# Kernel optimization log

Measured on AMD Instinct MI355X. Metric: run time of the kernel, lower is better.

Reference implementation:

```python
import jax, jax.numpy as jnp
import numpy as np
import math

B, S, HID, NH, HD = 2, 1024, 768, 12, 64
MAXP = 1024  # max_position_embeddings


def setup_inputs() -> dict:
    key = jax.random.key(0)
    ks = jax.random.split(key, 12)
    s = 0.02
    return {
        "hidden_states": jax.random.normal(ks[0], (B, S, HID), jnp.float32),
        "attention_mask": jnp.zeros((B, 1, 1, S), jnp.float32),
        "scaled_attention_mask": jax.random.uniform(ks[1], (1, 1, S, S), dtype=jnp.float32),
        "selector_outputs": jax.random.uniform(ks[2], (B, 1, S, 1), dtype=jnp.float32),
        "Wq": jax.random.normal(ks[3], (HID, HID), jnp.float32) * s,
        "bq": jnp.zeros((HID,), jnp.float32),
        "Wk": jax.random.normal(ks[4], (HID, HID), jnp.float32) * s,
        "bk": jnp.zeros((HID,), jnp.float32),
        "Wv": jax.random.normal(ks[5], (HID, HID), jnp.float32) * s,
        "bv": jnp.zeros((HID,), jnp.float32),
        "dist_emb": jax.random.normal(ks[6], (2 * MAXP - 1, HD), jnp.float32) * s,
    }


def _heads(x):
    # [B,S,HID] -> [B,NH,S,HD]
    return x.reshape(B, S, NH, HD).transpose(0, 2, 1, 3)


def reference(hidden_states, attention_mask, scaled_attention_mask, selector_outputs,
              Wq, bq, Wk, bk, Wv, bv, dist_emb):
    q = _heads(hidden_states @ Wq + bq)  # [B,NH,S,HD]
    k = _heads(hidden_states @ Wk + bk)
    v = _heads(hidden_states @ Wv + bv)

    scores = jnp.einsum('bhld,bhrd->bhlr', q, k)  # [B,NH,S,S]

    # relative_key positional bias
    pos = jnp.arange(S)
    dist_idx = pos[:, None] - pos[None, :] + (MAXP - 1)  # [S,S] in [0, 2*MAXP-2]
    pos_emb = dist_emb[dist_idx]  # [S,S,HD]
    scores = scores + jnp.einsum('bhld,lrd->bhlr', q, pos_emb)

    scores = scores / math.sqrt(HD)
    scores = scores + attention_mask  # additive mask (global branch)

    probs = jax.nn.softmax(scores, axis=-1)  # dropout prob = 0.0 -> identity
    context = jnp.einsum('bhlr,bhrd->bhld', probs, v)

    # local (selector-gated) branch; note: attention_mask added a second time,
    # faithful to the original code
    scores_l = scores * scaled_attention_mask + attention_mask
    probs_l = jax.nn.softmax(scores_l, axis=-1)
    local_context = jnp.einsum('bhlr,bhrd->bhld', probs_l, v)

    sel = selector_outputs  # [B,1,S,1]
    context = sel * local_context + (1.0 - sel) * context  # [B,NH,S,HD]

    # [B,NH,S,HD] -> [B,S,HID]
    return context.transpose(0, 2, 1, 3).reshape(B, S, HID)
```

## Files before the change

kernel.cpp:

```cpp
#include <hip/hip_runtime.h>
#include <hip/hip_bf16.h>
#include <math.h>

#define BB   2
#define SS   1024
#define HIDD 768
#define NHH  12
#define HDD  64

typedef float f32x4 __attribute__((ext_vector_type(4)));
typedef short bf8   __attribute__((ext_vector_type(8)));
typedef unsigned short u16;
typedef unsigned int u32;
typedef u16 u16x8 __attribute__((ext_vector_type(8)));
typedef u16 u16x4 __attribute__((ext_vector_type(4)));

__device__ __forceinline__ u16 f2bf(float x) {
  unsigned int u = __float_as_uint(x);
  u += 0x7fffu + ((u >> 16) & 1u);
  return (u16)(u >> 16);
}
__device__ __forceinline__ float bf2f(u16 x) {
  return __uint_as_float(((u32)x) << 16);
}

__device__ __forceinline__ bf8 ldfrag(const u16* t, int row, int kc) {
  return *(const bf8*)&t[row * 64 + (kc ^ ((row & 7) << 3))];
}

__global__ __launch_bounds__(256) void xconv_kernel(const float* __restrict__ X,
                                                    u16* __restrict__ Xb) {
  int i = (blockIdx.x * 256 + threadIdx.x) * 8;
  float4 a = *(const float4*)&X[i];
  float4 b = *(const float4*)&X[i + 4];
  u16x8 o;
  o[0] = f2bf(a.x); o[1] = f2bf(a.y); o[2] = f2bf(a.z); o[3] = f2bf(a.w);
  o[4] = f2bf(b.x); o[5] = f2bf(b.y); o[6] = f2bf(b.z); o[7] = f2bf(b.w);
  *(u16x8*)&Xb[i] = o;
}

__global__ __launch_bounds__(256) void wtconv_kernel(
    const float* __restrict__ Wq, const float* __restrict__ Wk,
    const float* __restrict__ Wv, u16* __restrict__ Wt) {
  const int zi = blockIdx.z;
  const float* __restrict__ W = (zi == 0) ? Wq : (zi == 1 ? Wk : Wv);
  const int n0 = blockIdx.x * 64;
  const int k0 = blockIdx.y * 64;
  __shared__ float t[64][65];
  const int tid = threadIdx.x;
  {
    const int kl = tid >> 4;
    const int nl = (tid & 15) * 4;
#pragma unroll
    for (int p = 0; p < 4; ++p) {
      float4 v = *(const float4*)&W[(size_t)(k0 + kl + 16 * p) * HIDD + n0 + nl];
      t[kl + 16 * p][nl + 0] = v.x;
      t[kl + 16 * p][nl + 1] = v.y;
      t[kl + 16 * p][nl + 2] = v.z;
      t[kl + 16 * p][nl + 3] = v.w;
    }
  }
  __syncthreads();
  {
    const int nl = tid >> 4;
    const int cl = (tid & 15) * 4;
#pragma unroll
    for (int p = 0; p < 4; ++p) {
      const int n = nl + 16 * p;
      u16x4 o;
      o[0] = f2bf(t[cl + 0][n]);
      o[1] = f2bf(t[cl + 1][n]);
      o[2] = f2bf(t[cl + 2][n]);
      o[3] = f2bf(t[cl + 3][n]);
      *(u16x4*)&Wt[(size_t)(zi * HIDD + n0 + n) * HIDD + k0 + cl] = o;
    }
  }
}

__global__ __launch_bounds__(256) void econv_kernel(const float* __restrict__ demb,
                                                    u16* __restrict__ eb) {
  int i = (blockIdx.x * 256 + threadIdx.x) * 8;
  if (i < 2047 * HDD) {
    float4 a = *(const float4*)&demb[i];
    float4 b = *(const float4*)&demb[i + 4];
    u16x8 o;
    o[0] = f2bf(a.x); o[1] = f2bf(a.y); o[2] = f2bf(a.z); o[3] = f2bf(a.w);
    o[4] = f2bf(b.x); o[5] = f2bf(b.y); o[6] = f2bf(b.z); o[7] = f2bf(b.w);
    *(u16x8*)&eb[i] = o;
  }
}

__global__ __launch_bounds__(256) void sconv_kernel(const float* __restrict__ sm,
                                                    u16* __restrict__ smb) {
  int i = (blockIdx.x * 256 + threadIdx.x) * 8;
  float4 a = *(const float4*)&sm[i];
  float4 b = *(const float4*)&sm[i + 4];
  u16x8 o;
  o[0] = f2bf(a.x); o[1] = f2bf(a.y); o[2] = f2bf(a.z); o[3] = f2bf(a.w);
  o[4] = f2bf(b.x); o[5] = f2bf(b.y); o[6] = f2bf(b.z); o[7] = f2bf(b.w);
  *(u16x8*)&smb[i] = o;
}

__global__ __launch_bounds__(256) void qkv_mfma_kernel(
    const u16* __restrict__ Xb,
    const u16* __restrict__ Wt,
    const float* __restrict__ bq, const float* __restrict__ bk,
    const float* __restrict__ bv,
    u16* __restrict__ qb, u16* __restrict__ kb, u16* __restrict__ vt) {
  const int bn = blockIdx.x;
  const int bm = blockIdx.y;
  const int zi = bn / 6;

  __shared__ u16 As[64 * 64];
  __shared__ u16 Bs[128 * 64];

  const int tid  = threadIdx.x;
  const int lane = tid & 63;
  const int w    = tid >> 6;
  const int g    = lane >> 4;
  const int ln   = lane & 15;
  const int wm   = (w >> 1) * 32;
  const int wn   = (w & 1) * 64;

  f32x4 acc[2][4] = {};

  const int srow = tid >> 3;
  const int scol = (tid & 7) * 8;
  const u16* Ag = Xb + (size_t)(bm * 64 + srow) * HIDD + scol;
  const u16* Bg = Wt + (size_t)(bn * 128 + srow) * HIDD + scol;

  for (int k0 = 0; k0 < HIDD; k0 += 64) {
    if (k0) __syncthreads();
#pragma unroll
    for (int p = 0; p < 2; ++p) {
      const int r = srow + 32 * p;
      const int sw = (r & 7) << 3;
      *(u16x8*)&As[r * 64 + (scol ^ sw)] =
          *(const u16x8*)&Ag[(size_t)(32 * p) * HIDD + k0];
    }
#pragma unroll
    for (int p = 0; p < 4; ++p) {
      const int r = srow + 32 * p;
      const int sw = (r & 7) << 3;
      *(u16x8*)&Bs[r * 64 + (scol ^ sw)] =
          *(const u16x8*)&Bg[(size_t)(32 * p) * HIDD + k0];
    }
    __syncthreads();

    bf8 af[2][2], bfr[4][2];
#pragma unroll
    for (int f = 0; f < 2; ++f)
#pragma unroll
      for (int kk = 0; kk < 2; ++kk)
        af[f][kk] = ldfrag(As, wm + 16 * f + ln, kk * 32 + g * 8);
#pragma unroll
    for (int f = 0; f < 4; ++f)
#pragma unroll
      for (int kk = 0; kk < 2; ++kk)
        bfr[f][kk] = ldfrag(Bs, wn + 16 * f + ln, kk * 32 + g * 8);
    if (zi < 2) {
#pragma unroll
      for (int mf = 0; mf < 2; ++mf)
#pragma unroll
        for (int nf = 0; nf < 4; ++nf)
#pragma unroll
          for (int kk = 0; kk < 2; ++kk)
            acc[mf][nf] = __builtin_amdgcn_mfma_f32_16x16x32_bf16(
                bfr[nf][kk], af[mf][kk], acc[mf][nf], 0, 0, 0);
    } else {
#pragma unroll
      for (int mf = 0; mf < 2; ++mf)
#pragma unroll
        for (int nf = 0; nf < 4; ++nf)
#pragma unroll
          for (int kk = 0; kk < 2; ++kk)
            acc[mf][nf] = __builtin_amdgcn_mfma_f32_16x16x32_bf16(
                af[mf][kk], bfr[nf][kk], acc[mf][nf], 0, 0, 0);
    }
  }

  const int mrow  = bm * 64 + wm;
  const int nbase = (bn % 6) * 128 + wn;
  const int h     = nbase >> 6;

  if (zi < 2) {
    const float* __restrict__ bias = zi ? bk : bq;
    u16* __restrict__ outp = zi ? kb : qb;
#pragma unroll
    for (int nf = 0; nf < 4; ++nf) {
      const int d0 = 16 * nf + 4 * g;
      float4 bi = *(const float4*)&bias[nbase + d0];
#pragma unroll
      for (int mf = 0; mf < 2; ++mf) {
        const int m = mrow + 16 * mf + ln;
        const int b = m >> 10, s = m & 1023;
        u16x4 o;
        o[0] = f2bf(acc[mf][nf][0] + bi.x);
        o[1] = f2bf(acc[mf][nf][1] + bi.y);
        o[2] = f2bf(acc[mf][nf][2] + bi.z);
        o[3] = f2bf(acc[mf][nf][3] + bi.w);
        *(u16x4*)&outp[(((size_t)(b * NHH + h)) * SS + s) * HDD + d0] = o;
      }
    }
  } else {
#pragma unroll
    for (int nf = 0; nf < 4; ++nf) {
      const int d = 16 * nf + ln;
      const float bi = bv[nbase + d];
#pragma unroll
      for (int mf = 0; mf < 2; ++mf) {
        const int m = mrow + 16 * mf + 4 * g;
        const int b = m >> 10, s = m & 1023;
        u16x4 o;
        o[0] = f2bf(acc[mf][nf][0] + bi);
        o[1] = f2bf(acc[mf][nf][1] + bi);
        o[2] = f2bf(acc[mf][nf][2] + bi);
        o[3] = f2bf(acc[mf][nf][3] + bi);
        *(u16x4*)&vt[(((size_t)(b * NHH + h)) * HDD + d) * SS + s] = o;
      }
    }
  }
}

__global__ __launch_bounds__(256, 3) void attn_kernel(
    const u16* __restrict__ qbg,
    const u16* __restrict__ kbg,
    const u16* __restrict__ vtg,
    const u16* __restrict__ eb,
    const float* __restrict__ am,
    const u16* __restrict__ smb,
    const float* __restrict__ selp,
    float* __restrict__ out) {
  const int bid  = blockIdx.x;
  const int xcd  = bid & 7;
  const int idx  = bid >> 3;
  const int inner = idx & 31;
  const int grp  = idx >> 5;
  const int hg   = grp * 8 + xcd;
  const int h    = hg % NHH;
  const int b    = hg / NHH;
  const int l0   = inner * 32;

  const int bh = b * NHH + h;
  const size_t hoff = (size_t)bh * SS * HDD;

  __shared__ __align__(16) u16 smbuf[16384];
  __shared__ __align__(4)  u16 tbuf[4 * 80 * 20];

  const int tid  = threadIdx.x;
  const int lane = tid & 63;
  const int w    = tid >> 6;
  const int p    = w >> 1;
  const int wp   = w & 1;
  const int g    = lane >> 4;
  const int ln   = lane & 15;

  u16* ksw = smbuf + p * 4096;
  u16* vsw = smbuf + 8192 + p * 4096;
  u16* Tw  = tbuf + w * (80 * 20);

  bf8 qf[2];
  {
    const u16* qp = qbg + hoff + (size_t)(l0 + 16 * wp + ln) * HDD + g * 8;
    qf[0] = *(const bf8*)(qp);
    qf[1] = *(const bf8*)(qp + 32);
  }

  f32x4 acc1[4] = {}, acc2[4] = {};
  float m1 = -INFINITY, m2 = -INFINITY, sum1 = 0.f, sum2 = 0.f;

  const int tid128 = tid & 127;
  const int rr = tid128 >> 2;
  const int cc = (tid128 & 3) << 4;
  const int S0i = ((lane & 16) << 1) | ln;
  const int S1i = S0i + 16;
  const bool ghi = (lane & 32) != 0;

  const u16* kgp0 = kbg + hoff;
  const u16* vgp0 = vtg + hoff;

  u16x8 kr[2][2], vr[2][2];
  {
    const int r0 = 512 * p;
#pragma unroll
    for (int pp = 0; pp < 2; ++pp) {
      const int r = rr + 32 * pp;
      kr[pp][0] = *(const u16x8*)&kgp0[(size_t)(r0 + r) * HDD + cc];
      kr[pp][1] = *(const u16x8*)&kgp0[(size_t)(r0 + r) * HDD + cc + 8];
      vr[pp][0] = *(const u16x8*)&vgp0[(size_t)r * SS + r0 + cc];
      vr[pp][1] = *(const u16x8*)&vgp0[(size_t)r * SS + r0 + cc + 8];
    }
  }

  for (int t = 0; t < 8; ++t) {
    const int r0 = 512 * p + 64 * t;

    const int W0 = l0 + 16 * wp - r0 + 960;
    bf8 ef[5][2];
#pragma unroll
    for (int c5 = 0; c5 < 5; ++c5) {
      const int gr = min(W0 + 16 * c5 + ln, 2046);
      const u16* ep = eb + (size_t)gr * HDD + g * 8;
      ef[c5][0] = *(const bf8*)(ep);
      ef[c5][1] = *(const bf8*)(ep + 32);
    }
    f32x4 amv[4];
    u16x4 smv[4];
#pragma unroll
    for (int ct = 0; ct < 4; ++ct) {
      amv[ct] = *(const f32x4*)&am[(b << 10) + r0 + 16 * ct + 4 * g];
      smv[ct] = *(const u16x4*)&smb[(size_t)(l0 + 16 * wp + ln) * SS +
                                    r0 + 16 * ct + 4 * g];
    }

    __syncthreads();
#pragma unroll
    for (int pp = 0; pp < 2; ++pp) {
      const int r = rr + 32 * pp;
      const int sw = (r & 7) << 3;
      *(u16x8*)&ksw[r * 64 + (cc ^ sw)] = kr[pp][0];
      *(u16x8*)&ksw[r * 64 + ((cc + 8) ^ sw)] = kr[pp][1];
      *(u16x8*)&vsw[r * 64 + (cc ^ sw)] = vr[pp][0];
      *(u16x8*)&vsw[r * 64 + ((cc + 8) ^ sw)] = vr[pp][1];
    }
    __syncthreads();

    if (t < 7) {
      const int rn = r0 + 64;
#pragma unroll
      for (int pp = 0; pp < 2; ++pp) {
        const int r = rr + 32 * pp;
        kr[pp][0] = *(const u16x8*)&kgp0[(size_t)(rn + r) * HDD + cc];
        kr[pp][1] = *(const u16x8*)&kgp0[(size_t)(rn + r) * HDD + cc + 8];
        vr[pp][0] = *(const u16x8*)&vgp0[(size_t)r * SS + rn + cc];
        vr[pp][1] = *(const u16x8*)&vgp0[(size_t)r * SS + rn + cc + 8];
      }
    }

    __builtin_amdgcn_s_setprio(1);
#pragma unroll
    for (int c5 = 0; c5 < 5; ++c5) {
      f32x4 x = {0.f, 0.f, 0.f, 0.f};
      x = __builtin_amdgcn_mfma_f32_16x16x32_bf16(ef[c5][0], qf[0], x, 0, 0, 0);
      x = __builtin_amdgcn_mfma_f32_16x16x32_bf16(ef[c5][1], qf[1], x, 0, 0, 0);
#pragma unroll
      for (int i = 0; i < 4; ++i)
        Tw[(16 * c5 + 4 * g + i) * 20 + ln] = f2bf(x[i]);
    }
    f32x4 sc[4];
#pragma unroll
    for (int ct = 0; ct < 4; ++ct) {
      f32x4 x = {0.f, 0.f, 0.f, 0.f};
#pragma unroll
      for (int kk = 0; kk < 2; ++kk)
        x = __builtin_amdgcn_mfma_f32_16x16x32_bf16(
            ldfrag(ksw, ct * 16 + ln, kk * 32 + g * 8), qf[kk], x, 0, 0, 0);
      sc[ct] = x;
    }
    __builtin_amdgcn_s_setprio(0);

    float s1r[4][4], s2r[4][4];
#pragma unroll
    for (int ct = 0; ct < 4; ++ct)
#pragma unroll
      for (int i = 0; i < 4; ++i) {
        const int e = ln + 63 - 16 * ct - 4 * g - i;
        const float tb = bf2f(Tw[e * 20 + ln]);
        const float s1 = (sc[ct][i] + tb) * 0.125f + amv[ct][i];
        s1r[ct][i] = s1;
        s2r[ct][i] = s1 * bf2f(smv[ct][i]) + amv[ct][i];
      }

    bf8 pa1[2], pa2[2];
    {
      float mx = s1r[0][0];
#pragma unroll
      for (int ct = 0; ct < 4; ++ct)
#pragma unroll
        for (int i = 0; i < 4; ++i) mx = fmaxf(mx, s1r[ct][i]);
      mx = fmaxf(mx, __shfl_xor(mx, 16, 64));
      mx = fmaxf(mx, __shfl_xor(mx, 32, 64));
      const float mn = fmaxf(m1, mx);
      const float scl = __expf(m1 - mn);
      m1 = mn;
      float rs = 0.f;
      u32 pk[4][2];
#pragma unroll
      for (int ct = 0; ct < 4; ++ct) {
        const float p0 = __expf(s1r[ct][0] - mn);
        const float p1 = __expf(s1r[ct][1] - mn);
        const float p2 = __expf(s1r[ct][2] - mn);
        const float p3 = __expf(s1r[ct][3] - mn);
        rs += (p0 + p1) + (p2 + p3);
        pk[ct][0] = (u32)f2bf(p0) | ((u32)f2bf(p1) << 16);
        pk[ct][1] = (u32)f2bf(p2) | ((u32)f2bf(p3) << 16);
      }
      rs += __shfl_xor(rs, 16, 64);
      rs += __shfl_xor(rs, 32, 64);
      sum1 = sum1 * scl + rs;
#pragma unroll
      for (int i = 0; i < 4; ++i) {
        const float s = __shfl(scl, (lane & 48) + 4 * g + i, 64);
#pragma unroll
        for (int dt = 0; dt < 4; ++dt) acc1[dt][i] *= s;
      }
#pragma unroll
      for (int kk = 0; kk < 2; ++kk) {
        union { u32 u[4]; bf8 v; } f;
        const int cA = 2 * kk, cB = 2 * kk + 1;
        u32 a, bb;
        a = (u32)__shfl((int)pk[cA][0], S0i, 64);
        bb = (u32)__shfl((int)pk[cB][0], S0i, 64);
        f.u[0] = ghi ? bb : a;
        a = (u32)__shfl((int)pk[cA][1], S0i, 64);
        bb = (u32)__shfl((int)pk[cB][1], S0i, 64);
        f.u[1] = ghi ? bb : a;
        a = (u32)__shfl((int)pk[cA][0], S1i, 64);
        bb = (u32)__shfl((int)pk[cB][0], S1i, 64);
        f.u[2] = ghi ? bb : a;
        a = (u32)__shfl((int)pk[cA][1], S1i, 64);
        bb = (u32)__shfl((int)pk[cB][1], S1i, 64);
        f.u[3] = ghi ? bb : a;
        pa1[kk] = f.v;
      }
    }
    {
      float mx = s2r[0][0];
#pragma unroll
      for (int ct = 0; ct < 4; ++ct)
#pragma unroll
        for (int i = 0; i < 4; ++i) mx = fmaxf(mx, s2r[ct][i]);
      mx = fmaxf(mx, __shfl_xor(mx, 16, 64));
      mx = fmaxf(mx, __shfl_xor(mx, 32, 64));
      const float mn = fmaxf(m2, mx);
      const float scl = __expf(m2 - mn);
      m2 = mn;
      float rs = 0.f;
      u32 pk[4][2];
#pragma unroll
      for (int ct = 0; ct < 4; ++ct) {
        const float p0 = __expf(s2r[ct][0] - mn);
        const float p1 = __expf(s2r[ct][1] - mn);
        const float p2 = __expf(s2r[ct][2] - mn);
        const float p3 = __expf(s2r[ct][3] - mn);
        rs += (p0 + p1) + (p2 + p3);
        pk[ct][0] = (u32)f2bf(p0) | ((u32)f2bf(p1) << 16);
        pk[ct][1] = (u32)f2bf(p2) | ((u32)f2bf(p3) << 16);
      }
      rs += __shfl_xor(rs, 16, 64);
      rs += __shfl_xor(rs, 32, 64);
      sum2 = sum2 * scl + rs;
#pragma unroll
      for (int i = 0; i < 4; ++i) {
        const float s = __shfl(scl, (lane & 48) + 4 * g + i, 64);
#pragma unroll
        for (int dt = 0; dt < 4; ++dt) acc2[dt][i] *= s;
      }
#pragma unroll
      for (int kk = 0; kk < 2; ++kk) {
        union { u32 u[4]; bf8 v; } f;
        const int cA = 2 * kk, cB = 2 * kk + 1;
        u32 a, bb;
        a = (u32)__shfl((int)pk[cA][0], S0i, 64);
        bb = (u32)__shfl((int)pk[cB][0], S0i, 64);
        f.u[0] = ghi ? bb : a;
        a = (u32)__shfl((int)pk[cA][1], S0i, 64);
        bb = (u32)__shfl((int)pk[cB][1], S0i, 64);
        f.u[1] = ghi ? bb : a;
        a = (u32)__shfl((int)pk[cA][0], S1i, 64);
        bb = (u32)__shfl((int)pk[cB][0], S1i, 64);
        f.u[2] = ghi ? bb : a;
        a = (u32)__shfl((int)pk[cA][1], S1i, 64);
        bb = (u32)__shfl((int)pk[cB][1], S1i, 64);
        f.u[3] = ghi ? bb : a;
        pa2[kk] = f.v;
      }
    }

    __builtin_amdgcn_s_setprio(1);
#pragma unroll
    for (int kk = 0; kk < 2; ++kk) {
#pragma unroll
      for (int dt = 0; dt < 4; ++dt) {
        bf8 vb = ldfrag(vsw, dt * 16 + ln, kk * 32 + g * 8);
        acc1[dt] = __builtin_amdgcn_mfma_f32_16x16x32_bf16(pa1[kk], vb, acc1[dt], 0, 0, 0);
        acc2[dt] = __builtin_amdgcn_mfma_f32_16x16x32_bf16(pa2[kk], vb, acc2[dt], 0, 0, 0);
      }
    }
    __builtin_amdgcn_s_setprio(0);
  }

  __syncthreads();
  float* scr = (float*)smbuf;
  if (p == 1) {
#pragma unroll
    for (int i = 0; i < 4; ++i) {
      const int row = 4 * g + i;
#pragma unroll
      for (int dt = 0; dt < 4; ++dt) {
        scr[wp * 1024 + row * 64 + dt * 16 + ln] = acc1[dt][i];
        scr[2048 + wp * 1024 + row * 64 + dt * 16 + ln] = acc2[dt][i];
      }
    }
    if (g == 0) {
      const int sb = 4096 + (wp * 16 + ln) * 4;
      scr[sb + 0] = m1;
      scr[sb + 1] = sum1;
      scr[sb + 2] = m2;
      scr[sb + 3] = sum2;
    }
  }
  __syncthreads();
  if (p == 0) {
    const int sb = 4096 + (wp * 16 + ln) * 4;
    const float mB1 = scr[sb + 0], sB1 = scr[sb + 1];
    const float mB2 = scr[sb + 2], sB2 = scr[sb + 3];
    const float M1 = fmaxf(m1, mB1);
    const float e1A = __expf(m1 - M1), e1B = __expf(mB1 - M1);
    const float inv1 = 1.f / (sum1 * e1A + sB1 * e1B);
    const float a1 = e1A * inv1, c1 = e1B * inv1;
    const float M2 = fmaxf(m2, mB2);
    const float e2A = __expf(m2 - M2), e2B = __expf(mB2 - M2);
    const float inv2 = 1.f / (sum2 * e2A + sB2 * e2B);
    const float a2 = e2A * inv2, c2 = e2B * inv2;
#pragma unroll
    for (int i = 0; i < 4; ++i) {
      const int src = (lane & 48) + 4 * g + i;
      const float a1s = __shfl(a1, src, 64), c1s = __shfl(c1, src, 64);
      const float a2s = __shfl(a2, src, 64), c2s = __shfl(c2, src, 64);
      const int row = 4 * g + i;
      const int lg = l0 + 16 * wp + row;
      const float se = selp[(b << 10) + lg];
#pragma unroll
      for (int dt = 0; dt < 4; ++dt) {
        const float aB1 = scr[wp * 1024 + row * 64 + dt * 16 + ln];
        const float aB2 = scr[2048 + wp * 1024 + row * 64 + dt * 16 + ln];
        const float o1 = acc1[dt][i] * a1s + aB1 * c1s;
        const float o2 = acc2[dt][i] * a2s + aB2 * c2s;
        out[((size_t)((b << 10) + lg)) * HIDD + h * HDD + dt * 16 + ln] =
            se * o2 + (1.f - se) * o1;
      }
    }
  }
}

extern "C" void kernel_launch(void* const* d_in, const int* in_sizes, int n_in,
                              void* d_out, int out_size, void* d_ws, size_t ws_size,
                              hipStream_t stream) {
  const float* hidden = (const float*)d_in[0];
  const float* am     = (const float*)d_in[1];
  const float* smask  = (const float*)d_in[2];
  const float* selp   = (const float*)d_in[3];
  const float* Wq     = (const float*)d_in[4];
  const float* bq     = (const float*)d_in[5];
  const float* Wk     = (const float*)d_in[6];
  const float* bk     = (const float*)d_in[7];
  const float* Wv     = (const float*)d_in[8];
  const float* bv     = (const float*)d_in[9];
  const float* demb   = (const float*)d_in[10];
  float* out = (float*)d_out;

  u16* wsp = (u16*)d_ws;
  const size_t NEL = (size_t)BB * NHH * SS * HDD;
  u16* Xb  = wsp;
  u16* Wt  = Xb + (size_t)2048 * HIDD;
  u16* qbw = Wt + (size_t)3 * HIDD * HIDD;
  u16* kbw = qbw + NEL;
  u16* vtw = kbw + NEL;
  u16* ebw = vtw + NEL;
  u16* smb = ebw + (size_t)2047 * HDD;

  xconv_kernel<<<768, 256, 0, stream>>>(hidden, Xb);
  dim3 gw(HIDD / 64, HIDD / 64, 3);
  wtconv_kernel<<<gw, 256, 0, stream>>>(Wq, Wk, Wv, Wt);
  econv_kernel<<<64, 256, 0, stream>>>(demb, ebw);
  sconv_kernel<<<512, 256, 0, stream>>>(smask, smb);

  dim3 g1(18, 32);
  qkv_mfma_kernel<<<g1, 256, 0, stream>>>(Xb, Wt, bq, bk, bv, qbw, kbw, vtw);

  attn_kernel<<<768, 256, 0, stream>>>(qbw, kbw, vtw, ebw, am, smb, selp, out);
}
```

Before: 105.5 us.

## Precompute relative-position bias in separate kernel and restructure attention with per-wave tiles

Moves the q·dist_emb relative-position bias into a separate tbias_kernel that writes a bf16 [B,NH,S,S] bias tensor to global memory. The attention kernel then streams that tensor instead of recomputing it with MFMAs. The attention kernel also changes: each wave gets its own private LDS K/V tiles of 32 keys, which removes the block-wide __syncthreads, and it register-prefetches the next tile. It adds a lazy softmax rescale that skips it when the running max grows by at most 8, and defers the row-sum shuffles to the end. The cost is an extra 48MB bias write and read through global memory.

Result: slower. 166.7 us (+58.0%).

```diff
diff --git a/kernel.cpp b/kernel.cpp
--- a/kernel.cpp
+++ b/kernel.cpp
@@ -222,11 +222,56 @@
   }
 }
 
+__global__ __launch_bounds__(256) void tbias_kernel(
+    const u16* __restrict__ qbg,
+    const u16* __restrict__ eb,
+    u16* __restrict__ Tg) {
+  const int bh = blockIdx.z;
+  const int l0 = blockIdx.y * 16;
+  const int tid = threadIdx.x;
+  const int lane = tid & 63;
+  const int w = tid >> 6;
+  const int g = lane >> 4;
+  const int ln = lane & 15;
+  const int r0 = (blockIdx.x * 4 + w) * 64;
+
+  __shared__ u16 tb[4][80 * 20];
+  u16* Tw = tb[w];
+
+  const u16* qp = qbg + ((size_t)bh * SS + l0 + ln) * HDD + g * 8;
+  const bf8 qf0 = *(const bf8*)qp;
+  const bf8 qf1 = *(const bf8*)(qp + 32);
+
+  const int W0 = l0 - r0 + 960;
+#pragma unroll
+  for (int c5 = 0; c5 < 5; ++c5) {
+    const int gr = min(max(W0 + 16 * c5 + ln, 0), 2046);
+    const u16* ep = eb + (size_t)gr * HDD + g * 8;
+    f32x4 x = {0.f, 0.f, 0.f, 0.f};
+    x = __builtin_amdgcn_mfma_f32_16x16x32_bf16(*(const bf8*)ep, qf0, x, 0, 0, 0);
+    x = __builtin_amdgcn_mfma_f32_16x16x32_bf16(*(const bf8*)(ep + 32), qf1, x, 0, 0, 0);
+#pragma unroll
+    for (int i = 0; i < 4; ++i)
+      Tw[(16 * c5 + 4 * g + i) * 20 + ln] = f2bf(x[i]);
+  }
+#pragma unroll
+  for (int ct = 0; ct < 4; ++ct) {
+    const int E0 = ln + 63 - 16 * ct - 4 * g;
+    u16x4 o;
+    o[0] = Tw[(E0 - 0) * 20 + ln];
+    o[1] = Tw[(E0 - 1) * 20 + ln];
+    o[2] = Tw[(E0 - 2) * 20 + ln];
+    o[3] = Tw[(E0 - 3) * 20 + ln];
+    __builtin_nontemporal_store(
+        o, (u16x4*)&Tg[((size_t)bh * SS + l0 + ln) * SS + r0 + 16 * ct + 4 * g]);
+  }
+}
+
 __global__ __launch_bounds__(256, 3) void attn_kernel(
     const u16* __restrict__ qbg,
     const u16* __restrict__ kbg,
     const u16* __restrict__ vtg,
-    const u16* __restrict__ eb,
+    const u16* __restrict__ Tg,
     const float* __restrict__ am,
     const u16* __restrict__ smb,
     const float* __restrict__ selp,
@@ -245,7 +290,6 @@
   const size_t hoff = (size_t)bh * SS * HDD;
 
   __shared__ __align__(16) u16 smbuf[16384];
-  __shared__ __align__(4)  u16 tbuf[4 * 80 * 20];
 
   const int tid  = threadIdx.x;
   const int lane = tid & 63;
@@ -255,101 +299,75 @@
   const int g    = lane >> 4;
   const int ln   = lane & 15;
 
-  u16* ksw = smbuf + p * 4096;
-  u16* vsw = smbuf + 8192 + p * 4096;
-  u16* Tw  = tbuf + w * (80 * 20);
-
+  u16* ksw = smbuf + w * 4096;
+  u16* vsw = ksw + 2048;
+
+  const int lq = l0 + 16 * wp + ln;
   bf8 qf[2];
   {
-    const u16* qp = qbg + hoff + (size_t)(l0 + 16 * wp + ln) * HDD + g * 8;
-    qf[0] = *(const bf8*)(qp);
+    const u16* qp = qbg + hoff + (size_t)lq * HDD + g * 8;
+    qf[0] = *(const bf8*)qp;
     qf[1] = *(const bf8*)(qp + 32);
   }
 
   f32x4 acc1[4] = {}, acc2[4] = {};
   float m1 = -INFINITY, m2 = -INFINITY, sum1 = 0.f, sum2 = 0.f;
 
-  const int tid128 = tid & 127;
-  const int rr = tid128 >> 2;
-  const int cc = (tid128 & 3) << 4;
-  const int S0i = ((lane & 16) << 1) | ln;
-  const int S1i = S0i + 16;
-  const bool ghi = (lane & 32) != 0;
-
-  const u16* kgp0 = kbg + hoff;
-  const u16* vgp0 = vtg + hoff;
-
-  u16x8 kr[2][2], vr[2][2];
+  const int srow = lane & 31;
+  const int sh   = (lane >> 5) * 32;
+  const int kx   = (srow & 7) << 3;
+  const int vrow = lane;
+  const int vx   = (vrow & 3) << 3;
+
+  const u16* kgp = kbg + hoff;
+  const u16* vgp = vtg + hoff + (size_t)vrow * SS;
+  const u16* Trow = Tg + ((size_t)bh * SS + lq) * SS;
+  const u16* Srow = smb + (size_t)lq * SS;
+  const float* Arow = am + (b << 10);
+
+  const int S0base = 16 * ((2 * g) & 3) + ln;
+  const int S1base = 16 * ((2 * g + 1) & 3) + ln;
+  const bool gh = (lane & 32) != 0;
+
+  u16x8 kq[4], vq[4];
+  u16x4 tbq[2], smq[2];
+  f32x4 amq[2];
   {
     const int r0 = 512 * p;
-#pragma unroll
-    for (int pp = 0; pp < 2; ++pp) {
-      const int r = rr + 32 * pp;
-      kr[pp][0] = *(const u16x8*)&kgp0[(size_t)(r0 + r) * HDD + cc];
-      kr[pp][1] = *(const u16x8*)&kgp0[(size_t)(r0 + r) * HDD + cc + 8];
-      vr[pp][0] = *(const u16x8*)&vgp0[(size_t)r * SS + r0 + cc];
-      vr[pp][1] = *(const u16x8*)&vgp0[(size_t)r * SS + r0 + cc + 8];
-    }
-  }
-
-  for (int t = 0; t < 8; ++t) {
-    const int r0 = 512 * p + 64 * t;
-
-    const int W0 = l0 + 16 * wp - r0 + 960;
-    bf8 ef[5][2];
-#pragma unroll
-    for (int c5 = 0; c5 < 5; ++c5) {
-      const int gr = min(W0 + 16 * c5 + ln, 2046);
-      const u16* ep = eb + (size_t)gr * HDD + g * 8;
-      ef[c5][0] = *(const bf8*)(ep);
-      ef[c5][1] = *(const bf8*)(ep + 32);
-    }
-    f32x4 amv[4];
-    u16x4 smv[4];
-#pragma unroll
-    for (int ct = 0; ct < 4; ++ct) {
-      amv[ct] = *(const f32x4*)&am[(b << 10) + r0 + 16 * ct + 4 * g];
-      smv[ct] = *(const u16x4*)&smb[(size_t)(l0 + 16 * wp + ln) * SS +
-                                    r0 + 16 * ct + 4 * g];
-    }
-
-    __syncthreads();
-#pragma unroll
-    for (int pp = 0; pp < 2; ++pp) {
-      const int r = rr + 32 * pp;
-      const int sw = (r & 7) << 3;
-      *(u16x8*)&ksw[r * 64 + (cc ^ sw)] = kr[pp][0];
-      *(u16x8*)&ksw[r * 64 + ((cc + 8) ^ sw)] = kr[pp][1];
-      *(u16x8*)&vsw[r * 64 + (cc ^ sw)] = vr[pp][0];
-      *(u16x8*)&vsw[r * 64 + ((cc + 8) ^ sw)] = vr[pp][1];
-    }
-    __syncthreads();
-
-    if (t < 7) {
-      const int rn = r0 + 64;
-#pragma unroll
-      for (int pp = 0; pp < 2; ++pp) {
-        const int r = rr + 32 * pp;
-        kr[pp][0] = *(const u16x8*)&kgp0[(size_t)(rn + r) * HDD + cc];
-        kr[pp][1] = *(const u16x8*)&kgp0[(size_t)(rn + r) * HDD + cc + 8];
-        vr[pp][0] = *(const u16x8*)&vgp0[(size_t)r * SS + rn + cc];
-        vr[pp][1] = *(const u16x8*)&vgp0[(size_t)r * SS + rn + cc + 8];
-      }
-    }
-
-    __builtin_amdgcn_s_setprio(1);
-#pragma unroll
-    for (int c5 = 0; c5 < 5; ++c5) {
-      f32x4 x = {0.f, 0.f, 0.f, 0.f};
-      x = __builtin_amdgcn_mfma_f32_16x16x32_bf16(ef[c5][0], qf[0], x, 0, 0, 0);
-      x = __builtin_amdgcn_mfma_f32_16x16x32_bf16(ef[c5][1], qf[1], x, 0, 0, 0);
-#pragma unroll
-      for (int i = 0; i < 4; ++i)
-        Tw[(16 * c5 + 4 * g + i) * 20 + ln] = f2bf(x[i]);
-    }
-    f32x4 sc[4];
-#pragma unroll
-    for (int ct = 0; ct < 4; ++ct) {
+    const u16* kg = kgp + (size_t)(r0 + srow) * HDD + sh;
+    kq[0] = *(const u16x8*)(kg + 0);
+    kq[1] = *(const u16x8*)(kg + 8);
+    kq[2] = *(const u16x8*)(kg + 16);
+    kq[3] = *(const u16x8*)(kg + 24);
+    const u16* vg = vgp + r0;
+    vq[0] = *(const u16x8*)(vg + 0);
+    vq[1] = *(const u16x8*)(vg + 8);
+    vq[2] = *(const u16x8*)(vg + 16);
+    vq[3] = *(const u16x8*)(vg + 24);
+#pragma unroll
+    for (int c = 0; c < 4; ++c) {
+      *(u16x8*)&ksw[srow * 64 + ((sh + 8 * c) ^ kx)] = kq[c];
+      *(u16x8*)&vsw[vrow * 32 + ((8 * c) ^ vx)] = vq[c];
+    }
+#pragma unroll
+    for (int ct = 0; ct < 2; ++ct) {
+      tbq[ct] = __builtin_nontemporal_load(
+          (const u16x4*)&Trow[r0 + 16 * ct + 4 * g]);
+      smq[ct] = *(const u16x4*)&Srow[r0 + 16 * ct + 4 * g];
+      amq[ct] = *(const f32x4*)&Arow[r0 + 16 * ct + 4 * g];
+    }
+  }
+
+  for (int t = 0; t < 16; ++t) {
+    const int r0 = 512 * p + 32 * t;
+
+    u16x4 tbv[2] = {tbq[0], tbq[1]};
+    u16x4 smv[2] = {smq[0], smq[1]};
+    f32x4 amv[2] = {amq[0], amq[1]};
+
+    f32x4 sc[2];
+#pragma unroll
+    for (int ct = 0; ct < 2; ++ct) {
       f32x4 x = {0.f, 0.f, 0.f, 0.f};
 #pragma unroll
       for (int kk = 0; kk < 2; ++kk)
@@ -357,138 +375,163 @@
             ldfrag(ksw, ct * 16 + ln, kk * 32 + g * 8), qf[kk], x, 0, 0, 0);
       sc[ct] = x;
     }
-    __builtin_amdgcn_s_setprio(0);
-
-    float s1r[4][4], s2r[4][4];
-#pragma unroll
-    for (int ct = 0; ct < 4; ++ct)
+    bf8 vbf[4];
+#pragma unroll
+    for (int dt = 0; dt < 4; ++dt)
+      vbf[dt] = *(const bf8*)&vsw[(16 * dt + ln) * 32 + 8 * (g ^ (ln & 3))];
+
+    if (t < 15) {
+      const int rn = r0 + 32;
+      const u16* kg = kgp + (size_t)(rn + srow) * HDD + sh;
+      kq[0] = *(const u16x8*)(kg + 0);
+      kq[1] = *(const u16x8*)(kg + 8);
+      kq[2] = *(const u16x8*)(kg + 16);
+      kq[3] = *(const u16x8*)(kg + 24);
+      const u16* vg = vgp + rn;
+      vq[0] = *(const u16x8*)(vg + 0);
+      vq[1] = *(const u16x8*)(vg + 8);
+      vq[2] = *(const u16x8*)(vg + 16);
+      vq[3] = *(const u16x8*)(vg + 24);
+#pragma unroll
+      for (int ct = 0; ct < 2; ++ct) {
+        tbq[ct] = __builtin_nontemporal_load(
+            (const u16x4*)&Trow[rn + 16 * ct + 4 * g]);
+        smq[ct] = *(const u16x4*)&Srow[rn + 16 * ct + 4 * g];
+        amq[ct] = *(const f32x4*)&Arow[rn + 16 * ct + 4 * g];
+      }
+    }
+
+    float s1r[2][4], s2r[2][4];
+#pragma unroll
+    for (int ct = 0; ct < 2; ++ct)
 #pragma unroll
       for (int i = 0; i < 4; ++i) {
-        const int e = ln + 63 - 16 * ct - 4 * g - i;
-        const float tb = bf2f(Tw[e * 20 + ln]);
-        const float s1 = (sc[ct][i] + tb) * 0.125f + amv[ct][i];
+        const float s1 = (sc[ct][i] + bf2f(tbv[ct][i])) * 0.125f + amv[ct][i];
         s1r[ct][i] = s1;
         s2r[ct][i] = s1 * bf2f(smv[ct][i]) + amv[ct][i];
       }
 
-    bf8 pa1[2], pa2[2];
+    bf8 pa1, pa2;
     {
-      float mx = s1r[0][0];
-#pragma unroll
-      for (int ct = 0; ct < 4; ++ct)
-#pragma unroll
-        for (int i = 0; i < 4; ++i) mx = fmaxf(mx, s1r[ct][i]);
-      mx = fmaxf(mx, __shfl_xor(mx, 16, 64));
-      mx = fmaxf(mx, __shfl_xor(mx, 32, 64));
-      const float mn = fmaxf(m1, mx);
-      const float scl = __expf(m1 - mn);
-      m1 = mn;
+      float pmax = s1r[0][0];
+#pragma unroll
+      for (int ct = 0; ct < 2; ++ct)
+#pragma unroll
+        for (int i = 0; i < 4; ++i) pmax = fmaxf(pmax, s1r[ct][i]);
+      if (!__all(pmax <= m1 + 8.f)) {
+        float mx = fmaxf(pmax, __shfl_xor(pmax, 16, 64));
+        mx = fmaxf(mx, __shfl_xor(mx, 32, 64));
+        const float mn = fmaxf(m1, mx);
+        const float scl = __expf(m1 - mn);
+        m1 = mn;
+        sum1 *= scl;
+#pragma unroll
+        for (int i = 0; i < 4; ++i) {
+          const float s = __shfl(scl, (lane & 48) + 4 * g + i, 64);
+#pragma unroll
+          for (int dt = 0; dt < 4; ++dt) acc1[dt][i] *= s;
+        }
+      }
+      u32 pk[2][2];
       float rs = 0.f;
-      u32 pk[4][2];
-#pragma unroll
-      for (int ct = 0; ct < 4; ++ct) {
-        const float p0 = __expf(s1r[ct][0] - mn);
-        const float p1 = __expf(s1r[ct][1] - mn);
-        const float p2 = __expf(s1r[ct][2] - mn);
-        const float p3 = __expf(s1r[ct][3] - mn);
+#pragma unroll
+      for (int ct = 0; ct < 2; ++ct) {
+        const float p0 = __expf(s1r[ct][0] - m1);
+        const float p1 = __expf(s1r[ct][1] - m1);
+        const float p2 = __expf(s1r[ct][2] - m1);
+        const float p3 = __expf(s1r[ct][3] - m1);
         rs += (p0 + p1) + (p2 + p3);
         pk[ct][0] = (u32)f2bf(p0) | ((u32)f2bf(p1) << 16);
         pk[ct][1] = (u32)f2bf(p2) | ((u32)f2bf(p3) << 16);
       }
-      rs += __shfl_xor(rs, 16, 64);
-      rs += __shfl_xor(rs, 32, 64);
-      sum1 = sum1 * scl + rs;
-#pragma unroll
-      for (int i = 0; i < 4; ++i) {
-        const float s = __shfl(scl, (lane & 48) + 4 * g + i, 64);
-#pragma unroll
-        for (int dt = 0; dt < 4; ++dt) acc1[dt][i] *= s;
-      }
-#pragma unroll
-      for (int kk = 0; kk < 2; ++kk) {
-        union { u32 u[4]; bf8 v; } f;
-        const int cA = 2 * kk, cB = 2 * kk + 1;
-        u32 a, bb;
-        a = (u32)__shfl((int)pk[cA][0], S0i, 64);
-        bb = (u32)__shfl((int)pk[cB][0], S0i, 64);
-        f.u[0] = ghi ? bb : a;
-        a = (u32)__shfl((int)pk[cA][1], S0i, 64);
-        bb = (u32)__shfl((int)pk[cB][1], S0i, 64);
-        f.u[1] = ghi ? bb : a;
-        a = (u32)__shfl((int)pk[cA][0], S1i, 64);
-        bb = (u32)__shfl((int)pk[cB][0], S1i, 64);
-        f.u[2] = ghi ? bb : a;
-        a = (u32)__shfl((int)pk[cA][1], S1i, 64);
-        bb = (u32)__shfl((int)pk[cB][1], S1i, 64);
-        f.u[3] = ghi ? bb : a;
-        pa1[kk] = f.v;
-      }
+      sum1 += rs;
+      union { u32 u[4]; bf8 v; } f;
+      u32 a, bb2;
+      a = (u32)__shfl((int)pk[0][0], S0base, 64);
+      bb2 = (u32)__shfl((int)pk[1][0], S0base, 64);
+      f.u[0] = gh ? bb2 : a;
+      a = (u32)__shfl((int)pk[0][1], S0base, 64);
+      bb2 = (u32)__shfl((int)pk[1][1], S0base, 64);
+      f.u[1] = gh ? bb2 : a;
+      a = (u32)__shfl((int)pk[0][0], S1base, 64);
+      bb2 = (u32)__shfl((int)pk[1][0], S1base, 64);
+      f.u[2] = gh ? bb2 : a;
+      a = (u32)__shfl((int)pk[0][1], S1base, 64);
+      bb2 = (u32)__shfl((int)pk[1][1], S1base, 64);
+      f.u[3] = gh ? bb2 : a;
+      pa1 = f.v;
     }
     {
-      float mx = s2r[0][0];
-#pragma unroll
-      for (int ct = 0; ct < 4; ++ct)
-#pragma unroll
-        for (int i = 0; i < 4; ++i) mx = fmaxf(mx, s2r[ct][i]);
-      mx = fmaxf(mx, __shfl_xor(mx, 16, 64));
-      mx = fmaxf(mx, __shfl_xor(mx, 32, 64));
-      const float mn = fmaxf(m2, mx);
-      const float scl = __expf(m2 - mn);
-      m2 = mn;
+      float pmax = s2r[0][0];
+#pragma unroll
+      for (int ct = 0; ct < 2; ++ct)
+#pragma unroll
+        for (int i = 0; i < 4; ++i) pmax = fmaxf(pmax, s2r[ct][i]);
+      if (!__all(pmax <= m2 + 8.f)) {
+        float mx = fmaxf(pmax, __shfl_xor(pmax, 16, 64));
+        mx = fmaxf(mx, __shfl_xor(mx, 32, 64));
+        const float mn = fmaxf(m2, mx);
+        const float scl = __expf(m2 - mn);
+        m2 = mn;
+        sum2 *= scl;
+#pragma unroll
+        for (int i = 0; i < 4; ++i) {
+          const float s = __shfl(scl, (lane & 48) + 4 * g + i, 64);
+#pragma unroll
+          for (int dt = 0; dt < 4; ++dt) acc2[dt][i] *= s;
+        }
+      }
+      u32 pk[2][2];
       float rs = 0.f;
-      u32 pk[4][2];
-#pragma unroll
-      for (int ct = 0; ct < 4; ++ct) {
-        const float p0 = __expf(s2r[ct][0] - mn);
-        const float p1 = __expf(s2r[ct][1] - mn);
-        const float p2 = __expf(s2r[ct][2] - mn);
-        const float p3 = __expf(s2r[ct][3] - mn);
+#pragma unroll
+      for (int ct = 0; ct < 2; ++ct) {
+        const float p0 = __expf(s2r[ct][0] - m2);
+        const float p1 = __expf(s2r[ct][1] - m2);
+        const float p2 = __expf(s2r[ct][2] - m2);
+        const float p3 = __expf(s2r[ct][3] - m2);
         rs += (p0 + p1) + (p2 + p3);
         pk[ct][0] = (u32)f2bf(p0) | ((u32)f2bf(p1) << 16);
         pk[ct][1] = (u32)f2bf(p2) | ((u32)f2bf(p3) << 16);
       }
-      rs += __shfl_xor(rs, 16, 64);
-      rs += __shfl_xor(rs, 32, 64);
-      sum2 = sum2 * scl + rs;
-#pragma unroll
-      for (int i = 0; i < 4; ++i) {
-        const float s = __shfl(scl, (lane & 48) + 4 * g + i, 64);
-#pragma unroll
-        for (int dt = 0; dt < 4; ++dt) acc2[dt][i] *= s;
-      }
-#pragma unroll
-      for (int kk = 0; kk < 2; ++kk) {
-        union { u32 u[4]; bf8 v; } f;
-        const int cA = 2 * kk, cB = 2 * kk + 1;
-        u32 a, bb;
-        a = (u32)__shfl((int)pk[cA][0], S0i, 64);
-        bb = (u32)__shfl((int)pk[cB][0], S0i, 64);
-        f.u[0] = ghi ? bb : a;
-        a = (u32)__shfl((int)pk[cA][1], S0i, 64);
-        bb = (u32)__shfl((int)pk[cB][1], S0i, 64);
-        f.u[1] = ghi ? bb : a;
-        a = (u32)__shfl((int)pk[cA][0], S1i, 64);
-        bb = (u32)__shfl((int)pk[cB][0], S1i, 64);
-        f.u[2] = ghi ? bb : a;
-        a = (u32)__shfl((int)pk[cA][1], S1i, 64);
-        bb = (u32)__shfl((int)pk[cB][1], S1i, 64);
-        f.u[3] = ghi ? bb : a;
-        pa2[kk] = f.v;
+      sum2 += rs;
+      union { u32 u[4]; bf8 v; } f;
+      u32 a, bb2;
+      a = (u32)__shfl((int)pk[0][0], S0base, 64);
+      bb2 = (u32)__shfl((int)pk[1][0], S0base, 64);
+      f.u[0] = gh ? bb2 : a;
+      a = (u32)__shfl((int)pk[0][1], S0base, 64);
+      bb2 = (u32)__shfl((int)pk[1][1], S0base, 64);
+      f.u[1] = gh ? bb2 : a;
+      a = (u32)__shfl((int)pk[0][0], S1base, 64);
+      bb2 = (u32)__shfl((int)pk[1][0], S1base, 64);
+      f.u[2] = gh ? bb2 : a;
+      a = (u32)__shfl((int)pk[0][1], S1base, 64);
+      bb2 = (u32)__shfl((int)pk[1][1], S1base, 64);
+      f.u[3] = gh ? bb2 : a;
+      pa2 = f.v;
+    }
+
+    if (t < 15) {
+#pragma unroll
+      for (int c = 0; c < 4; ++c) {
+        *(u16x8*)&ksw[srow * 64 + ((sh + 8 * c) ^ kx)] = kq[c];
+        *(u16x8*)&vsw[vrow * 32 + ((8 * c) ^ vx)] = vq[c];
       }
     }
 
     __builtin_amdgcn_s_setprio(1);
 #pragma unroll
-    for (int kk = 0; kk < 2; ++kk) {
-#pragma unroll
-      for (int dt = 0; dt < 4; ++dt) {
-        bf8 vb = ldfrag(vsw, dt * 16 + ln, kk * 32 + g * 8);
-        acc1[dt] = __builtin_amdgcn_mfma_f32_16x16x32_bf16(pa1[kk], vb, acc1[dt], 0, 0, 0);
-        acc2[dt] = __builtin_amdgcn_mfma_f32_16x16x32_bf16(pa2[kk], vb, acc2[dt], 0, 0, 0);
-      }
+    for (int dt = 0; dt < 4; ++dt) {
+      acc1[dt] = __builtin_amdgcn_mfma_f32_16x16x32_bf16(pa1, vbf[dt], acc1[dt], 0, 0, 0);
+      acc2[dt] = __builtin_amdgcn_mfma_f32_16x16x32_bf16(pa2, vbf[dt], acc2[dt], 0, 0, 0);
     }
     __builtin_amdgcn_s_setprio(0);
   }
+
+  sum1 += __shfl_xor(sum1, 16, 64);
+  sum1 += __shfl_xor(sum1, 32, 64);
+  sum2 += __shfl_xor(sum2, 16, 64);
+  sum2 += __shfl_xor(sum2, 32, 64);
 
   __syncthreads();
   float* scr = (float*)smbuf;
@@ -569,6 +612,7 @@
   u16* vtw = kbw + NEL;
   u16* ebw = vtw + NEL;
   u16* smb = ebw + (size_t)2047 * HDD;
+  u16* Tgw = smb + (size_t)SS * SS;
 
   xconv_kernel<<<768, 256, 0, stream>>>(hidden, Xb);
   dim3 gw(HIDD / 64, HIDD / 64, 3);
@@ -579,5 +623,8 @@
   dim3 g1(18, 32);
   qkv_mfma_kernel<<<g1, 256, 0, stream>>>(Xb, Wt, bq, bk, bv, qbw, kbw, vtw);
 
-  attn_kernel<<<768, 256, 0, stream>>>(qbw, kbw, vtw, ebw, am, smb, selp, out);
-}
+  dim3 gt(4, 64, BB * NHH);
+  tbias_kernel<<<gt, 256, 0, stream>>>(qbw, ebw, Tgw);
+
+  attn_kernel<<<768, 256, 0, stream>>>(qbw, kbw, vtw, Tgw, am, smb, selp, out);
+}
```
